# Kernel optimization log

Hardware: AMD Instinct MI355X
Metric: run time of the kernel (lower is better)

Reference implementation:

```python
import jax, jax.numpy as jnp
import numpy as np

B, I, O, N = 65536, 256, 32, 8


def chebyshev_basis(x, n):
    """Chebyshev polynomials T_0..T_{n-1} of x. x: [B, I] -> [B, I, n]."""
    T = [jnp.ones_like(x), x]
    for _ in range(n - 2):
        T.append(2.0 * x * T[-1] - T[-2])
    return jnp.stack(T[:n], axis=-1)


def setup_inputs() -> dict:
    key = jax.random.key(0)
    k1, k2 = jax.random.split(key)
    # inputs live on [-1, 1], the natural Chebyshev domain
    x = jax.random.uniform(k1, (B, I), jnp.float32, minval=-1.0, maxval=1.0)
    # weight init mirrors torch: uniform(-weight_magnitude/in, weight_magnitude/in)
    w = jax.random.uniform(k2, (O, I, N), jnp.float32, minval=-1.0 / I, maxval=1.0 / I)
    return {"x": x, "w": w}


def reference(x, w):
    n = w.shape[-1]
    phi = chebyshev_basis(x, n)          # [B, I, n] basis expansion
    out = jnp.einsum("bin,oin->bo", phi, w)  # weighted contraction
    return out
```

## Files before the change

### kernel.cpp

```cpp
#include <hip/hip_runtime.h>
#include <hip/hip_bf16.h>


typedef __attribute__((ext_vector_type(8)))  short bf16x8;
typedef __attribute__((ext_vector_type(16))) float f32x16;
typedef __attribute__((ext_vector_type(4)))  float f32x4;

__device__ __forceinline__ short f2b(float f) {
    __hip_bfloat16 h = __float2bfloat16(f);
    short s;
    __builtin_memcpy(&s, &h, sizeof(s));
    return s;
}

__global__ __launch_bounds__(256) void prep_w_kernel(const float* __restrict__ w,
                                                     short* __restrict__ wB) {
    int idx = blockIdx.x * 256 + threadIdx.x;
    int kc2 = idx >> 9;
    int l   = (idx >> 3) & 63;
    int jj  = idx & 7;
    int o = l & 31, g = l >> 5;
    int i = 2 * kc2 + (jj >> 2);
    int n = 4 * g + (jj & 3);
    wB[idx] = f2b(w[(o * 256 + i) * 8 + n]);
}

__global__ __launch_bounds__(256, 5) void cheb_mm_kernel(const float* __restrict__ x,
                                                         const short* __restrict__ wB,
                                                         float* __restrict__ out) {
    __shared__ float smem[8192];
    const int tid = threadIdx.x;
    const int wv  = tid >> 6;
    const int l   = tid & 63;
    const int g   = l >> 5;
    const int r0  = l & 31;
    const long long rowB = (long long)blockIdx.x * 32;

    {
        const float4* xg4 = (const float4*)(x + rowB * 256);
        float4 stg[8];
        #pragma unroll
        for (int q = 0; q < 8; ++q)
            stg[q] = xg4[q * 256 + tid];
        float2* s2 = (float2*)smem;
        #pragma unroll
        for (int q = 0; q < 8; ++q) {
            int slot = q * 256 + tid;
            int row = slot >> 6, f4 = slot & 63;
            int p0 = 2 * f4, p1 = 2 * f4 + 1;
            int d0 = (p0 & ~31) + ((p0 & 31) ^ (row & 31));
            int d1 = (p1 & ~31) + ((p1 & 31) ^ (row & 31));
            s2[row * 128 + d0] = make_float2(stg[q].x, stg[q].y);
            s2[row * 128 + d1] = make_float2(stg[q].z, stg[q].w);
        }
    }
    __syncthreads();

    f32x16 acc{};
    const bf16x8* wBv = (const bf16x8*)wB;
    const float2* srow = (const float2*)smem + r0 * 128 + wv * 32;

    #pragma unroll 8
    for (int t = 0; t < 32; ++t) {
        const bf16x8 bfrag = wBv[(wv * 32 + t) * 64 + l];
        const float2 xv = srow[t ^ r0];
        const float xa = xv.x, xb = xv.y;
        const float x2a = xa + xa, x2b = xb + xb;
        const float a2 = x2a * xa - 1.f;
        const float a3 = x2a * a2 - xa;
        const float a4 = x2a * a3 - a2;
        const float a5 = x2a * a4 - a3;
        const float b2 = x2b * xb - 1.f;
        const float b3 = x2b * b2 - xb;
        const float b4 = x2b * b3 - b2;
        const float b5 = x2b * b4 - b3;
        const float ua0 = g ? a4 : 1.f;
        const float ua1 = g ? a5 : xa;
        const float ua2 = x2a * ua1 - ua0;
        const float ua3 = x2a * ua2 - ua1;
        const float ub0 = g ? b4 : 1.f;
        const float ub1 = g ? b5 : xb;
        const float ub2 = x2b * ub1 - ub0;
        const float ub3 = x2b * ub2 - ub1;
        bf16x8 afrag;
        afrag[0] = f2b(ua0); afrag[1] = f2b(ua1);
        afrag[2] = f2b(ua2); afrag[3] = f2b(ua3);
        afrag[4] = f2b(ub0); afrag[5] = f2b(ub1);
        afrag[6] = f2b(ub2); afrag[7] = f2b(ub3);
        acc = __builtin_amdgcn_mfma_f32_32x32x16_bf16(afrag, bfrag, acc, 0, 0, 0);
    }

    __syncthreads();
    #pragma unroll
    for (int r = 0; r < 16; ++r) {
        const int rloc = (r & 3) + 8 * (r >> 2) + 4 * g;
        smem[wv * 1024 + rloc * 32 + r0] = acc[r];
    }
    __syncthreads();

    {
        float* op = out + rowB * 32;
        const int f = tid * 4;
        f32x4 v0 = *(const f32x4*)&smem[f];
        f32x4 v1 = *(const f32x4*)&smem[1024 + f];
        f32x4 v2 = *(const f32x4*)&smem[2048 + f];
        f32x4 v3 = *(const f32x4*)&smem[3072 + f];
        f32x4 s = (v0 + v1) + (v2 + v3);
        *(f32x4*)(op + f) = s;
    }
}

extern "C" void kernel_launch(void* const* d_in, const int* in_sizes, int n_in,
                              void* d_out, int out_size, void* d_ws, size_t ws_size,
                              hipStream_t stream) {
    const float* x = (const float*)d_in[0];
    const float* w = (const float*)d_in[1];
    float* out = (float*)d_out;
    short* wB = (short*)d_ws;

    prep_w_kernel<<<256, 256, 0, stream>>>(w, wB);
    cheb_mm_kernel<<<2048, 256, 0, stream>>>(x, wB, out);
}
```

Measured before the change: 33.76 us.

## Compute full Chebyshev recurrence per lane and exchange halves via permlane32_swap

Each lane now reads a single x value and computes T0..T7 once, instead of each half-wave computing overlapping recurrences for two x values. The permlane32_swap builtin redistributes the packed bf16 pairs into the MFMA A-fragment layout, and conversion uses a packed two-value bf16 convert. It also software-prefetches the weight fragments and x values into a register ring, and splits accumulation across two accumulators so consecutive MFMAs do not depend on each other. The cost is extra cross-lane ops, more registers for the prefetch buffers, and a fallback path selected by __has_builtin.

```diff
diff --git a/kernel.cpp b/kernel.cpp
--- a/kernel.cpp
+++ b/kernel.cpp
@@ -11,6 +11,13 @@
     short s;
     __builtin_memcpy(&s, &h, sizeof(s));
     return s;
+}
+
+__device__ __forceinline__ unsigned pkbf(float lo, float hi) {
+    __hip_bfloat162 h2 = __float22bfloat162_rn(make_float2(lo, hi));
+    unsigned u;
+    __builtin_memcpy(&u, &h2, 4);
+    return u;
 }
 
 __global__ __launch_bounds__(256) void prep_w_kernel(const float* __restrict__ w,
@@ -56,13 +63,52 @@
     }
     __syncthreads();
 
-    f32x16 acc{};
-    const bf16x8* wBv = (const bf16x8*)wB;
+    f32x16 accA{}, accB{};
+    const bf16x8* wq = (const bf16x8*)wB + wv * 2048 + l;
+    const float* sf = smem;
+    const int xbase = r0 * 256 + wv * 64 + g;
+
+#if __has_builtin(__builtin_amdgcn_permlane32_swap)
+    bf16x8 bfc[4];
+    float  xc[2];
+    #pragma unroll
+    for (int p = 0; p < 4; ++p) bfc[p] = wq[p * 64];
+    xc[0] = sf[xbase + ((0 ^ r0) << 1)];
+    xc[1] = sf[xbase + ((1 ^ r0) << 1)];
+
+    #pragma unroll
+    for (int t = 0; t < 32; ++t) {
+        const bf16x8 bfrag = bfc[t & 3];
+        const float  xv    = xc[t & 1];
+        if (t + 4 < 32) bfc[t & 3] = wq[(t + 4) * 64];
+        if (t + 2 < 32) xc[t & 1] = sf[xbase + (((t + 2) ^ r0) << 1)];
+
+        const float x2 = xv + xv;
+        const float T2 = fmaf(x2, xv, -1.f);
+        const float T3 = fmaf(x2, T2, -xv);
+        const float T4 = fmaf(x2, T3, -T2);
+        const float T5 = fmaf(x2, T4, -T3);
+        const float T6 = fmaf(x2, T5, -T4);
+        const float T7 = fmaf(x2, T6, -T5);
+        unsigned R0 = pkbf(1.f, xv);
+        unsigned R1 = pkbf(T2, T3);
+        unsigned R2 = pkbf(T4, T5);
+        unsigned R3 = pkbf(T6, T7);
+        auto r02 = __builtin_amdgcn_permlane32_swap(R0, R2, false, false);
+        auto r13 = __builtin_amdgcn_permlane32_swap(R1, R3, false, false);
+        union { unsigned u[4]; bf16x8 v; } af;
+        af.u[0] = r02[0]; af.u[1] = r13[0];
+        af.u[2] = r02[1]; af.u[3] = r13[1];
+        if (t & 1)
+            accB = __builtin_amdgcn_mfma_f32_32x32x16_bf16(af.v, bfrag, accB, 0, 0, 0);
+        else
+            accA = __builtin_amdgcn_mfma_f32_32x32x16_bf16(af.v, bfrag, accA, 0, 0, 0);
+    }
+#else
     const float2* srow = (const float2*)smem + r0 * 128 + wv * 32;
-
     #pragma unroll 8
     for (int t = 0; t < 32; ++t) {
-        const bf16x8 bfrag = wBv[(wv * 32 + t) * 64 + l];
+        const bf16x8 bfrag = wq[t * 64];
         const float2 xv = srow[t ^ r0];
         const float xa = xv.x, xb = xv.y;
         const float x2a = xa + xa, x2b = xb + xb;
@@ -87,8 +133,13 @@
         afrag[2] = f2b(ua2); afrag[3] = f2b(ua3);
         afrag[4] = f2b(ub0); afrag[5] = f2b(ub1);
         afrag[6] = f2b(ub2); afrag[7] = f2b(ub3);
-        acc = __builtin_amdgcn_mfma_f32_32x32x16_bf16(afrag, bfrag, acc, 0, 0, 0);
+        if (t & 1)
+            accB = __builtin_amdgcn_mfma_f32_32x32x16_bf16(afrag, bfrag, accB, 0, 0, 0);
+        else
+            accA = __builtin_amdgcn_mfma_f32_32x32x16_bf16(afrag, bfrag, accA, 0, 0, 0);
     }
+#endif
+    const f32x16 acc = accA + accB;
 
     __syncthreads();
     #pragma unroll
```

Result: faster. 32.24 us (-4.5%).
